# Kernel optimization log

Measured on AMD Instinct MI355X. Metric: run time of the kernel, lower is better.

The kernel has to match this reference:

```python
import jax, jax.numpy as jnp
import numpy as np

DIM = 64      # input/output channels
DIM_K = 16    # key/query dim k
HEADS = 4     # h
U = 1         # intra-depth u
V = DIM // HEADS  # per-head value dim = 16
M = 14        # global context size (D = H = W = M)
REL = 2 * M - 1   # 27
EPS = 1e-5


def _rel_indices(m):
    # positions [n,3], n = m^3; rel_pos[i,j] = pos[j] - pos[i], clamp, shift
    g = np.meshgrid(np.arange(m), np.arange(m), np.arange(m), indexing='ij')
    pos = np.stack(g, axis=-1).reshape(-1, 3)                 # [n,3]
    rel = pos[None, :, :] - pos[:, None, :]                   # [n,n,3]
    rel = np.clip(rel, -m, m) + (m - 1)
    return rel[..., 0], rel[..., 1], rel[..., 2]              # each [n,n]

_D_IDX, _H_IDX, _W_IDX = _rel_indices(M)


def _batchnorm(t, gamma, beta):
    # BatchNorm3d, training mode: per-channel batch stats over (B, D, H, W)
    mean = jnp.mean(t, axis=(0, 2, 3, 4), keepdims=True)
    var = jnp.var(t, axis=(0, 2, 3, 4), keepdims=True)
    tn = (t - mean) * jax.lax.rsqrt(var + EPS)
    return tn * gamma[None, :, None, None, None] + beta[None, :, None, None, None]


def setup_inputs() -> dict:
    key = jax.random.key(0)
    ks = jax.random.split(key, 6)
    B = 4
    x = jax.random.normal(ks[0], (B, DIM, M, M, M), dtype=jnp.float32)
    # 1x1x1 convs == channel matmuls, weight [out_ch, in_ch]
    Wq = jax.random.normal(ks[1], (DIM_K * HEADS, DIM), dtype=jnp.float32) * (DIM_K * DIM) ** (-0.5)
    Wk = jax.random.normal(ks[2], (DIM_K * U, DIM), dtype=jnp.float32) * DIM ** (-0.5)
    Wv = jax.random.normal(ks[3], (V * U, DIM), dtype=jnp.float32) * DIM ** (-0.5)
    rel_pos_emb = jax.random.uniform(ks[4], (REL, REL, REL, DIM_K, U), dtype=jnp.float32)
    gamma_q = jnp.ones((DIM_K * HEADS,), dtype=jnp.float32)
    beta_q = jnp.zeros((DIM_K * HEADS,), dtype=jnp.float32)
    gamma_v = jnp.ones((V * U,), dtype=jnp.float32)
    beta_v = jnp.zeros((V * U,), dtype=jnp.float32)
    return {"x": x, "Wq": Wq, "Wk": Wk, "Wv": Wv, "rel_pos_emb": rel_pos_emb,
            "gamma_q": gamma_q, "beta_q": beta_q, "gamma_v": gamma_v, "beta_v": beta_v}


def reference(x, Wq, Wk, Wv, rel_pos_emb, gamma_q, beta_q, gamma_v, beta_v):
    B, C, D, H, W = x.shape
    n = D * H * W
    q = jnp.einsum('oc,bcdhw->bodhw', Wq, x)
    k = jnp.einsum('oc,bcdhw->bodhw', Wk, x)
    v = jnp.einsum('oc,bcdhw->bodhw', Wv, x)
    q = _batchnorm(q, gamma_q, beta_q)
    v = _batchnorm(v, gamma_v, beta_v)
    q = q.reshape(B, HEADS, DIM_K, n)     # b h k n
    k = k.reshape(B, U, DIM_K, n)         # b u k m
    v = v.reshape(B, U, V, n)             # b u v m
    k = jax.nn.softmax(k, axis=-1)
    # content lambda
    lambda_c = jnp.einsum('bukm,buvm->bkv', k, v)
    y_c = jnp.einsum('bhkn,bkv->bhvn', q, lambda_c)
    # positional lambda via relative-position embedding gather
    rpe = rel_pos_emb[_D_IDX, _H_IDX, _W_IDX]          # [n, n, k, u]
    lambda_p = jnp.einsum('nmku,buvm->bnkv', rpe, v)   # [b, n, k, v]
    y_p = jnp.einsum('bhkn,bnkv->bhvn', q, lambda_p)
    Y = y_c + y_p                                       # [b, h, v, n]
    return Y.reshape(B, HEADS * V, D, H, W)
```

## Files before the change

kernel.cpp:

```cpp
#include <hip/hip_runtime.h>
#include <hip/hip_bf16.h>

#define NPOS 2744
#define BB 4
#define BNTOT (BB*NPOS)
#define RELVOL 19683
#define EROWS2 19688
#define NRT 196
#define NV2 (NRT*2*64)
#define N4T 1024
#define NGRP3 29
#define WDW3 5220

typedef __bf16 bf16x8 __attribute__((ext_vector_type(8)));
typedef float f32x16 __attribute__((ext_vector_type(16)));

#define WS_Q  0u
#define WS_K  2809856u
#define WS_V  3512320u
#define WS_ST 4214784u
#define WS_LA 4216192u
#define WS_LC 4220544u
#define WS_E2 4224640u
#define WS_LP 4856704u
#define WS_VF WS_K

__device__ inline unsigned short f2bf(float f) {
  unsigned int u = __float_as_uint(f);
  return (unsigned short)((u + 0x7fffu + ((u >> 16) & 1u)) >> 16);
}
__device__ inline unsigned int fsh(unsigned int hi, unsigned int lo, int shbits) {
  return (unsigned int)(((((unsigned long long)hi) << 32) | lo) >> shbits);
}
__device__ inline unsigned int pk2(float a, float b) {
  return (unsigned int)f2bf(a) | ((unsigned int)f2bf(b) << 16);
}
__device__ inline float ubf(unsigned int d, int hf) {
  return __uint_as_float(((d >> hf) & 0xFFFFu) << 16);
}

__global__ __launch_bounds__(256) void k_qkv(const float* __restrict__ x,
    const float* __restrict__ Wq, const float* __restrict__ Wk, const float* __restrict__ Wv,
    const float* __restrict__ rpe,
    float* __restrict__ qws, float* __restrict__ kws, float* __restrict__ vws,
    unsigned short* __restrict__ ebf, float* __restrict__ la) {
  int bid = blockIdx.x;
  int tid = threadIdx.x;
  if (bid >= 516) {
    int bid2 = bid - 516;
    if (bid2 == 0 && tid < 272) ((float4*)la)[tid] = make_float4(0.f, 0.f, 0.f, 0.f);
    const int TOT = 16 * EROWS2 + 1024;
    for (int e = bid2 * 256 + tid; e < TOT; e += 308 * 256) {
      if (e < 16 * EROWS2) {
        int k = e / EROWS2;
        int i = e - k * EROWS2;
        float val = (i < RELVOL) ? rpe[i * 16 + k] : 0.f;
        ebf[e] = f2bf(val);
      } else {
        ebf[e] = 0;
      }
    }
    return;
  }
  int cg = bid % 12, nb = bid / 12;
  int gid = nb * 256 + tid;
  if (gid >= BNTOT) return;
  int b = gid / NPOS, n = gid - b * NPOS;
  const float* xp = x + (size_t)b * 64 * NPOS + n;
  int ch0 = cg * 8;
  const float* wbase;
  float* obase;
  if (ch0 < 64)      { wbase = Wq + ch0 * 64;        obase = qws + ((size_t)b * 64 + ch0) * NPOS + n; }
  else if (ch0 < 80) { wbase = Wk + (ch0 - 64) * 64; obase = kws + ((size_t)b * 16 + (ch0 - 64)) * NPOS + n; }
  else               { wbase = Wv + (ch0 - 80) * 64; obase = vws + ((size_t)b * 16 + (ch0 - 80)) * NPOS + n; }

  float acc[8];
#pragma unroll
  for (int j = 0; j < 8; ++j) acc[j] = 0.f;
  for (int c = 0; c < 64; c += 4) {
    float x0 = xp[(c + 0) * NPOS], x1 = xp[(c + 1) * NPOS];
    float x2 = xp[(c + 2) * NPOS], x3 = xp[(c + 3) * NPOS];
#pragma unroll
    for (int j = 0; j < 8; ++j) {
      float4 w = *(const float4*)(wbase + j * 64 + c);
      acc[j] += w.x * x0 + w.y * x1 + w.z * x2 + w.w * x3;
    }
  }
#pragma unroll
  for (int j = 0; j < 8; ++j) obase[(size_t)j * NPOS] = acc[j];
}

__global__ __launch_bounds__(256) void k_sl(const float* __restrict__ qws,
    const float* __restrict__ kws, const float* __restrict__ vws,
    const float* __restrict__ gq, const float* __restrict__ bq,
    const float* __restrict__ gv, const float* __restrict__ bv,
    float* __restrict__ st, float* __restrict__ lcacc) {
  int bid = blockIdx.x;
  int tid = threadIdx.x;
  int wid = tid >> 6;
  __shared__ float red[17][4];
  if (bid < 80) {
    int ch = bid;
    const float* p = (ch < 64) ? (qws + (size_t)ch * NPOS) : (vws + (size_t)(ch - 64) * NPOS);
    size_t pstride = (ch < 64) ? (size_t)64 * NPOS : (size_t)16 * NPOS;
    float s = 0.f, ss = 0.f;
    for (int b = 0; b < 4; ++b) {
      const float* pp = p + b * pstride;
      for (int n = tid; n < NPOS; n += 256) { float v = pp[n]; s += v; ss += v * v; }
    }
#pragma unroll
    for (int o = 32; o > 0; o >>= 1) { s += __shfl_xor(s, o, 64); ss += __shfl_xor(ss, o, 64); }
    if ((tid & 63) == 0) { red[0][wid] = s; red[1][wid] = ss; }
    __syncthreads();
    if (tid == 0) {
      float S = red[0][0] + red[0][1] + red[0][2] + red[0][3];
      float SS = red[1][0] + red[1][1] + red[1][2] + red[1][3];
      float mean = S / (float)BNTOT;
      float var = SS / (float)BNTOT - mean * mean;
      float inv = rsqrtf(var + 1e-5f);
      float g, be;
      if (ch < 64) { g = gq[ch]; be = bq[ch]; } else { g = gv[ch - 64]; be = bv[ch - 64]; }
      float sc = g * inv, sh = be - mean * sc;
      if (ch < 64) { st[ch] = sc; st[64 + ch] = sh; }
      else { st[128 + (ch - 64)] = sc; st[144 + (ch - 64)] = sh; }
    }
  } else {
    int bid2 = bid - 80;
    int b = bid2 >> 6, kc = (bid2 >> 2) & 15, seg = bid2 & 3;
    const float* kp = kws + ((size_t)b * 16 + kc) * NPOS;
    const float* vp = vws + (size_t)b * 16 * NPOS;
    float s = 0.f, acc[16];
#pragma unroll
    for (int v = 0; v < 16; ++v) acc[v] = 0.f;
    int m0 = seg * 686;
    for (int m = m0 + tid; m < m0 + 686; m += 256) {
      float e = __expf(kp[m]);
      s += e;
#pragma unroll
      for (int v = 0; v < 16; ++v) acc[v] += e * vp[(size_t)v * NPOS + m];
    }
#pragma unroll
    for (int o = 32; o > 0; o >>= 1) {
      s += __shfl_xor(s, o, 64);
#pragma unroll
      for (int v = 0; v < 16; ++v) acc[v] += __shfl_xor(acc[v], o, 64);
    }
    if ((tid & 63) == 0) { red[16][wid] = s; for (int v = 0; v < 16; ++v) red[v][wid] = acc[v]; }
    __syncthreads();
    if (tid < 17) {
      float tot = red[tid][0] + red[tid][1] + red[tid][2] + red[tid][3];
      atomicAdd(lcacc + ((size_t)b * 16 + kc) * 17 + tid, tot);
    }
  }
}

__global__ __launch_bounds__(256) void k_conv2(const float* __restrict__ vws,
    const float* __restrict__ st, const float* __restrict__ lcacc,
    uint4* __restrict__ vfrag, float* __restrict__ lc) {
  int idx = blockIdx.x * 256 + threadIdx.x;
  if (idx < NV2) {
    int rt = idx >> 7; int r = idx & 127;
    int ct = r >> 6, l = r & 63;
    int zm = rt / 14, ym = rt - zm * 14;
    int kh = l >> 5;
    int b = ct * 2 + ((l >> 4) & 1), v = l & 15;
    int mrow = zm * 196 + ym * 14;
    float sc = st[128 + v], sh = st[144 + v];
    unsigned int wds[4];
#pragma unroll
    for (int i = 0; i < 4; ++i) {
      int x0 = kh * 8 + 2 * i, x1 = x0 + 1;
      float f0 = 0.f, f1 = 0.f;
      if (x0 < 14) f0 = vws[((size_t)b * 16 + v) * NPOS + mrow + x0] * sc + sh;
      if (x1 < 14) f1 = vws[((size_t)b * 16 + v) * NPOS + mrow + x1] * sc + sh;
      wds[i] = (unsigned int)f2bf(f0) | ((unsigned int)f2bf(f1) << 16);
    }
    vfrag[(rt * 2 + ct) * 64 + l] = make_uint4(wds[0], wds[1], wds[2], wds[3]);
  } else if (idx < NV2 + N4T) {
    int t = idx - NV2;
    int b = t >> 8, kc = (t >> 4) & 15, v = t & 15;
    const float* la = lcacc + ((size_t)b * 16 + kc) * 17;
    float S = la[16];
    lc[((size_t)b * 16 + kc) * 16 + v] = st[128 + v] * (la[v] / S) + st[144 + v];
  }
}

__global__ __launch_bounds__(256, 3) void k_lam(const unsigned short* __restrict__ ebf,
    const uint4* __restrict__ vfrag, unsigned int* __restrict__ lpb) {
  __shared__ unsigned int lds[12320];
  int tid = threadIdx.x;
  int w = tid >> 6, l = tid & 63;
  int bid = blockIdx.x;
  int k = bid / NGRP3, ng = bid - k * NGRP3;
  int n0 = ng * 96;
  int nmax = min(n0 + 95, NPOS - 1);
  int zx = nmax / 196, tx = nmax - zx * 196, yx = tx / 14, xx = tx - yx * 14;
  int b0 = (9841 - (zx * 729 + yx * 27 + xx)) & ~7;

  const unsigned int* gsrc = (const unsigned int*)(ebf + (size_t)k * EROWS2 + b0);
#pragma unroll
  for (int it = 0; it < 6; ++it) {
    int ck = it * 256 + tid;
    if (ck < WDW3 / 4) {
      uint4 g = *(const uint4*)(gsrc + 4 * ck);
      unsigned int g4 = gsrc[4 * ck + 4];
      *(uint4*)(&lds[4 * ck]) = g;
      uint4 h;
      h.x = fsh(g.y, g.x, 16); h.y = fsh(g.z, g.y, 16);
      h.z = fsh(g.w, g.z, 16); h.w = fsh(g4, g.w, 16);
      *(uint4*)(&lds[WDW3 + 4 * ck]) = h;
    }
  }
  int i = l & 31, kh = l >> 5;
  int n_a = min(n0 + i, NPOS - 1);
  int n_b = min(n0 + 32 + i, NPOS - 1);
  int n_c = min(n0 + 64 + i, NPOS - 1);
  int za = n_a / 196, ta = n_a - za * 196, ya = ta / 14, xa = ta - ya * 14;
  int zb = n_b / 196, tb = n_b - zb * 196, yb = tb / 14, xb = tb - yb * 14;
  int zc = n_c / 196, tc = n_c - zc * 196, yc = tc / 14, xc = tc - yc * 14;
  int soff0 = 9841 - (za * 729 + ya * 27 + xa) - b0 + kh * 8;
  int soff1 = 9841 - (zb * 729 + yb * 27 + xb) - b0 + kh * 8;
  int soff2 = 9841 - (zc * 729 + yc * 27 + xc) - b0 + kh * 8;
  __syncthreads();

  f32x16 a0c0, a0c1, a1c0, a1c1, a2c0, a2c1;
#pragma unroll
  for (int q = 0; q < 16; ++q) {
    a0c0[q] = 0.f; a0c1[q] = 0.f; a1c0[q] = 0.f;
    a1c1[q] = 0.f; a2c0[q] = 0.f; a2c1[q] = 0.f;
  }

  int rtS = w * 49;
  int zm = rtS / 14, ym = rtS - zm * 14;
  int crel = zm * 729 + ym * 27;
  const uint4* vfp = vfrag + (size_t)(rtS * 2) * 64 + l;
  uint4 B0 = vfp[0], B1 = vfp[64];
  for (int d = 0; d < 49; ++d) {
    const uint4* vfn = vfp + ((d < 48) ? 128 : 0);
    uint4 nB0 = vfn[0], nB1 = vfn[64];
    int o0 = soff0 + crel, o1 = soff1 + crel, o2 = soff2 + crel;
    int ad0 = (o0 >> 1) + (o0 & 1) * WDW3;
    int ad1 = (o1 >> 1) + (o1 & 1) * WDW3;
    int ad2 = (o2 >> 1) + (o2 & 1) * WDW3;
    uint4 A0 = make_uint4(lds[ad0], lds[ad0 + 1], lds[ad0 + 2], lds[ad0 + 3]);
    uint4 A1 = make_uint4(lds[ad1], lds[ad1 + 1], lds[ad1 + 2], lds[ad1 + 3]);
    uint4 A2 = make_uint4(lds[ad2], lds[ad2 + 1], lds[ad2 + 2], lds[ad2 + 3]);
    __builtin_amdgcn_s_setprio(1);
    a0c0 = __builtin_amdgcn_mfma_f32_32x32x16_bf16(
        __builtin_bit_cast(bf16x8, A0), __builtin_bit_cast(bf16x8, B0), a0c0, 0, 0, 0);
    a0c1 = __builtin_amdgcn_mfma_f32_32x32x16_bf16(
        __builtin_bit_cast(bf16x8, A0), __builtin_bit_cast(bf16x8, B1), a0c1, 0, 0, 0);
    a1c0 = __builtin_amdgcn_mfma_f32_32x32x16_bf16(
        __builtin_bit_cast(bf16x8, A1), __builtin_bit_cast(bf16x8, B0), a1c0, 0, 0, 0);
    a1c1 = __builtin_amdgcn_mfma_f32_32x32x16_bf16(
        __builtin_bit_cast(bf16x8, A1), __builtin_bit_cast(bf16x8, B1), a1c1, 0, 0, 0);
    a2c0 = __builtin_amdgcn_mfma_f32_32x32x16_bf16(
        __builtin_bit_cast(bf16x8, A2), __builtin_bit_cast(bf16x8, B0), a2c0, 0, 0, 0);
    a2c1 = __builtin_amdgcn_mfma_f32_32x32x16_bf16(
        __builtin_bit_cast(bf16x8, A2), __builtin_bit_cast(bf16x8, B1), a2c1, 0, 0, 0);
    __builtin_amdgcn_s_setprio(0);
    B0 = nB0; B1 = nB1; vfp = vfn;
    ++ym;
    if (ym == 14) { ym = 0; crel += 378; } else { crel += 27; }
  }

  __syncthreads();
  float* red = (float*)lds;
  if (w >= 2) {
    float* r0 = red + (w - 2) * 6144;
#pragma unroll
    for (int r = 0; r < 16; ++r) {
      r0[r * 64 + l] = a0c0[r];          r0[1024 + r * 64 + l] = a0c1[r];
      r0[2048 + r * 64 + l] = a1c0[r];   r0[3072 + r * 64 + l] = a1c1[r];
      r0[4096 + r * 64 + l] = a2c0[r];   r0[5120 + r * 64 + l] = a2c1[r];
    }
  }
  __syncthreads();
  if (w < 2) {
    const float* r0 = red + w * 6144;
#pragma unroll
    for (int r = 0; r < 16; ++r) {
      a0c0[r] += r0[r * 64 + l];         a0c1[r] += r0[1024 + r * 64 + l];
      a1c0[r] += r0[2048 + r * 64 + l];  a1c1[r] += r0[3072 + r * 64 + l];
      a2c0[r] += r0[4096 + r * 64 + l];  a2c1[r] += r0[5120 + r * 64 + l];
    }
  }
  __syncthreads();
  if (w == 1) {
#pragma unroll
    for (int r = 0; r < 16; ++r) {
      red[r * 64 + l] = a0c0[r];          red[1024 + r * 64 + l] = a0c1[r];
      red[2048 + r * 64 + l] = a1c0[r];   red[3072 + r * 64 + l] = a1c1[r];
      red[4096 + r * 64 + l] = a2c0[r];   red[5120 + r * 64 + l] = a2c1[r];
    }
  }
  __syncthreads();
  if (w == 0) {
#pragma unroll
    for (int r = 0; r < 16; ++r) {
      a0c0[r] += red[r * 64 + l];         a0c1[r] += red[1024 + r * 64 + l];
      a1c0[r] += red[2048 + r * 64 + l];  a1c1[r] += red[3072 + r * 64 + l];
      a2c0[r] += red[4096 + r * 64 + l];  a2c1[r] += red[5120 + r * 64 + l];
    }
    float* fl = (float*)lds;
    int bv0 = ((l >> 4) & 1) * 16 + (l & 15);
#define DUMP(ACC, NT, CT)                                                   \
    {                                                                       \
_Pragma("unroll")                                                           \
      for (int r = 0; r < 16; ++r) {                                        \
        int nl = (NT) * 32 + ((r & 3) + 8 * (r >> 2) + 4 * kh);             \
        fl[nl * 64 + (CT) * 32 + bv0] = ACC[r];                             \
      }                                                                     \
    }
    DUMP(a0c0, 0, 0) DUMP(a0c1, 0, 1)
    DUMP(a1c0, 1, 0) DUMP(a1c1, 1, 1)
    DUMP(a2c0, 2, 0) DUMP(a2c1, 2, 1)
#undef DUMP
  }
  __syncthreads();
  {
    const float* fl = (const float*)lds;
#pragma unroll
    for (int it = 0; it < 12; ++it) {
      int idx = it * 256 + tid;
      int vd = idx & 7, b = (idx >> 3) & 3, nl = idx >> 5;
      int n = n0 + nl;
      if (n < NPOS) {
        float2 f = *(const float2*)&fl[nl * 64 + b * 16 + 2 * vd];
        lpb[((size_t)(b * NPOS + n) * 16 + k) * 8 + vd] = pk2(f.x, f.y);
      }
    }
  }
}

__global__ __launch_bounds__(128) void k_ep(const unsigned int* __restrict__ lpb,
    const float* __restrict__ qws, const float* __restrict__ st,
    const float* __restrict__ lc, float* __restrict__ out) {
  __shared__ unsigned int laml[32 * 130];
  __shared__ float qlds[64 * 33];
  __shared__ float lclds[256];
  int tid = threadIdx.x;
  int bid = blockIdx.x;
  int b = bid & 3, chk = bid >> 2;
  int n0 = chk * 32;
  const uint4* lsrc = (const uint4*)(lpb + (size_t)(b * NPOS + n0) * 128);
#pragma unroll
  for (int it = 0; it < 8; ++it) {
    int idx4 = it * 128 + tid;
    uint4 g = lsrc[idx4];
    int n_loc = idx4 >> 5, rem = (idx4 & 31) * 4;
    unsigned int* d = &laml[n_loc * 130 + rem];
    d[0] = g.x; d[1] = g.y; d[2] = g.z; d[3] = g.w;
  }
  const float* qb = qws + (size_t)b * 64 * NPOS + n0;
#pragma unroll
  for (int it = 0; it < 4; ++it) {
    int idx4 = it * 128 + tid;
    int ch = idx4 >> 3, c4 = (idx4 & 7) * 4;
    float4 g = *(const float4*)(qb + (size_t)ch * NPOS + c4);
    float sc = st[ch], sh = st[64 + ch];
    float* d = &qlds[ch * 33 + c4];
    d[0] = g.x * sc + sh; d[1] = g.y * sc + sh;
    d[2] = g.z * sc + sh; d[3] = g.w * sc + sh;
  }
  lclds[tid] = lc[b * 256 + tid];
  lclds[128 + tid] = lc[b * 256 + 128 + tid];
  __syncthreads();
  int vq = tid & 3, n_loc = tid >> 2;
  int n = n0 + n_loc;
  if (n >= NPOS) return;
  float y[16];
#pragma unroll
  for (int i = 0; i < 16; ++i) y[i] = 0.f;
#pragma unroll
  for (int k = 0; k < 16; ++k) {
    uint2 lp = *(const uint2*)&laml[n_loc * 130 + k * 8 + vq * 2];
    const float* lcr = &lclds[k * 16 + vq * 4];
    float l0 = ubf(lp.x, 0) + lcr[0];
    float l1 = ubf(lp.x, 16) + lcr[1];
    float l2 = ubf(lp.y, 0) + lcr[2];
    float l3 = ubf(lp.y, 16) + lcr[3];
#pragma unroll
    for (int h = 0; h < 4; ++h) {
      float q = qlds[(h * 16 + k) * 33 + n_loc];
      y[h * 4 + 0] += q * l0; y[h * 4 + 1] += q * l1;
      y[h * 4 + 2] += q * l2; y[h * 4 + 3] += q * l3;
    }
  }
  size_t ob = ((size_t)b * 64 + vq * 4) * NPOS + n;
#pragma unroll
  for (int h = 0; h < 4; ++h)
#pragma unroll
    for (int j = 0; j < 4; ++j)
      out[ob + (size_t)(h * 16 + j) * NPOS] = y[h * 4 + j];
}

extern "C" void kernel_launch(void* const* d_in, const int* in_sizes, int n_in,
                              void* d_out, int out_size, void* d_ws, size_t ws_size,
                              hipStream_t stream) {
  const float* x   = (const float*)d_in[0];
  const float* Wq  = (const float*)d_in[1];
  const float* Wk  = (const float*)d_in[2];
  const float* Wv  = (const float*)d_in[3];
  const float* rpe = (const float*)d_in[4];
  const float* gq  = (const float*)d_in[5];
  const float* bq  = (const float*)d_in[6];
  const float* gv  = (const float*)d_in[7];
  const float* bv  = (const float*)d_in[8];
  float* out = (float*)d_out;
  char* ws = (char*)d_ws;
  float* qws = (float*)(ws + WS_Q);
  float* kws = (float*)(ws + WS_K);
  float* vws = (float*)(ws + WS_V);
  float* st  = (float*)(ws + WS_ST);
  float* la  = (float*)(ws + WS_LA);
  float* lcp = (float*)(ws + WS_LC);
  unsigned short* ebf = (unsigned short*)(ws + WS_E2);
  unsigned int* lpb = (unsigned int*)(ws + WS_LP);
  uint4* vfrag = (uint4*)(ws + WS_VF);

  k_qkv<<<824, 256, 0, stream>>>(x, Wq, Wk, Wv, rpe, qws, kws, vws, ebf, la);
  k_sl<<<336, 256, 0, stream>>>(qws, kws, vws, gq, bq, gv, bv, st, la);
  k_conv2<<<102, 256, 0, stream>>>(vws, st, la, vfrag, lcp);
  k_lam<<<16 * NGRP3, 256, 0, stream>>>(ebf, vfrag, lpb);
  k_ep<<<344, 128, 0, stream>>>(lpb, qws, st, lcp, out);
}
```

Before: 60.92 us.

## Split k_lam reduction over m into two halves with smaller n tiles

k_lam now tiles n by 64 instead of 96 and splits the m (source position) range into two halves handled by separate blocks. Each block stages a smaller LDS window of the embedding, which allows 4 blocks per CU and 1376 blocks instead of 464. Block ids are remapped in an XCD-aware order. The two partial lambda_p results are written to separate halves of the workspace as bf16 and summed in k_ep. This adds an extra bf16 rounding step and doubles lpb traffic in exchange for more parallelism and occupancy.

```diff
diff --git a/kernel.cpp b/kernel.cpp
--- a/kernel.cpp
+++ b/kernel.cpp
@@ -9,8 +9,9 @@
 #define NRT 196
 #define NV2 (NRT*2*64)
 #define N4T 1024
-#define NGRP3 29
-#define WDW3 5220
+#define NGRP 43
+#define WDWH 2688
+#define HALFDW ((size_t)4*NPOS*16*8)
 
 typedef __bf16 bf16x8 __attribute__((ext_vector_type(8)));
 typedef float f32x16 __attribute__((ext_vector_type(16)));
@@ -37,6 +38,9 @@
 }
 __device__ inline float ubf(unsigned int d, int hf) {
   return __uint_as_float(((d >> hf) & 0xFFFFu) << 16);
+}
+__device__ inline unsigned int addpk(unsigned int a, unsigned int b) {
+  return pk2(ubf(a, 0) + ubf(b, 0), ubf(a, 16) + ubf(b, 16));
 }
 
 __global__ __launch_bounds__(256) void k_qkv(const float* __restrict__ x,
@@ -185,79 +189,72 @@
   }
 }
 
-__global__ __launch_bounds__(256, 3) void k_lam(const unsigned short* __restrict__ ebf,
+__global__ __launch_bounds__(256, 4) void k_lam(const unsigned short* __restrict__ ebf,
     const uint4* __restrict__ vfrag, unsigned int* __restrict__ lpb) {
-  __shared__ unsigned int lds[12320];
+  __shared__ unsigned int lds[5412];
   int tid = threadIdx.x;
   int w = tid >> 6, l = tid & 63;
-  int bid = blockIdx.x;
-  int k = bid / NGRP3, ng = bid - k * NGRP3;
-  int n0 = ng * 96;
-  int nmax = min(n0 + 95, NPOS - 1);
+  int orig = blockIdx.x;
+  int bid = (orig & 7) * 172 + (orig >> 3);
+  int mh = bid & 1, kb = bid >> 1;
+  int k = kb / NGRP, ng = kb - k * NGRP;
+  int n0 = ng * 64;
+  int crowbase = 5103 * mh;
+  int nmax = min(n0 + 63, NPOS - 1);
   int zx = nmax / 196, tx = nmax - zx * 196, yx = tx / 14, xx = tx - yx * 14;
-  int b0 = (9841 - (zx * 729 + yx * 27 + xx)) & ~7;
+  int b0 = (9841 - (zx * 729 + yx * 27 + xx) + crowbase) & ~7;
 
   const unsigned int* gsrc = (const unsigned int*)(ebf + (size_t)k * EROWS2 + b0);
 #pragma unroll
-  for (int it = 0; it < 6; ++it) {
+  for (int it = 0; it < 3; ++it) {
     int ck = it * 256 + tid;
-    if (ck < WDW3 / 4) {
+    if (ck < WDWH / 4) {
       uint4 g = *(const uint4*)(gsrc + 4 * ck);
       unsigned int g4 = gsrc[4 * ck + 4];
       *(uint4*)(&lds[4 * ck]) = g;
       uint4 h;
       h.x = fsh(g.y, g.x, 16); h.y = fsh(g.z, g.y, 16);
       h.z = fsh(g.w, g.z, 16); h.w = fsh(g4, g.w, 16);
-      *(uint4*)(&lds[WDW3 + 4 * ck]) = h;
+      *(uint4*)(&lds[WDWH + 4 * ck]) = h;
     }
   }
   int i = l & 31, kh = l >> 5;
   int n_a = min(n0 + i, NPOS - 1);
   int n_b = min(n0 + 32 + i, NPOS - 1);
-  int n_c = min(n0 + 64 + i, NPOS - 1);
   int za = n_a / 196, ta = n_a - za * 196, ya = ta / 14, xa = ta - ya * 14;
   int zb = n_b / 196, tb = n_b - zb * 196, yb = tb / 14, xb = tb - yb * 14;
-  int zc = n_c / 196, tc = n_c - zc * 196, yc = tc / 14, xc = tc - yc * 14;
-  int soff0 = 9841 - (za * 729 + ya * 27 + xa) - b0 + kh * 8;
-  int soff1 = 9841 - (zb * 729 + yb * 27 + xb) - b0 + kh * 8;
-  int soff2 = 9841 - (zc * 729 + yc * 27 + xc) - b0 + kh * 8;
+  int soff0 = 9841 - (za * 729 + ya * 27 + xa) + crowbase - b0 + kh * 8;
+  int soff1 = 9841 - (zb * 729 + yb * 27 + xb) + crowbase - b0 + kh * 8;
   __syncthreads();
 
-  f32x16 a0c0, a0c1, a1c0, a1c1, a2c0, a2c1;
-#pragma unroll
-  for (int q = 0; q < 16; ++q) {
-    a0c0[q] = 0.f; a0c1[q] = 0.f; a1c0[q] = 0.f;
-    a1c1[q] = 0.f; a2c0[q] = 0.f; a2c1[q] = 0.f;
-  }
-
-  int rtS = w * 49;
+  f32x16 ac00, ac01, ac10, ac11;
+#pragma unroll
+  for (int q = 0; q < 16; ++q) { ac00[q] = 0.f; ac01[q] = 0.f; ac10[q] = 0.f; ac11[q] = 0.f; }
+
+  const int stw[5] = {0, 25, 50, 74, 98};
+  int rtS = mh * 98 + stw[w];
+  int cnt = stw[w + 1] - stw[w];
   int zm = rtS / 14, ym = rtS - zm * 14;
-  int crel = zm * 729 + ym * 27;
+  int crel = (zm - 7 * mh) * 729 + ym * 27;
   const uint4* vfp = vfrag + (size_t)(rtS * 2) * 64 + l;
   uint4 B0 = vfp[0], B1 = vfp[64];
-  for (int d = 0; d < 49; ++d) {
-    const uint4* vfn = vfp + ((d < 48) ? 128 : 0);
+  for (int d = 0; d < cnt; ++d) {
+    const uint4* vfn = vfp + ((d < cnt - 1) ? 128 : 0);
     uint4 nB0 = vfn[0], nB1 = vfn[64];
-    int o0 = soff0 + crel, o1 = soff1 + crel, o2 = soff2 + crel;
-    int ad0 = (o0 >> 1) + (o0 & 1) * WDW3;
-    int ad1 = (o1 >> 1) + (o1 & 1) * WDW3;
-    int ad2 = (o2 >> 1) + (o2 & 1) * WDW3;
+    int o0 = soff0 + crel, o1 = soff1 + crel;
+    int ad0 = (o0 >> 1) + (o0 & 1) * WDWH;
+    int ad1 = (o1 >> 1) + (o1 & 1) * WDWH;
     uint4 A0 = make_uint4(lds[ad0], lds[ad0 + 1], lds[ad0 + 2], lds[ad0 + 3]);
     uint4 A1 = make_uint4(lds[ad1], lds[ad1 + 1], lds[ad1 + 2], lds[ad1 + 3]);
-    uint4 A2 = make_uint4(lds[ad2], lds[ad2 + 1], lds[ad2 + 2], lds[ad2 + 3]);
     __builtin_amdgcn_s_setprio(1);
-    a0c0 = __builtin_amdgcn_mfma_f32_32x32x16_bf16(
-        __builtin_bit_cast(bf16x8, A0), __builtin_bit_cast(bf16x8, B0), a0c0, 0, 0, 0);
-    a0c1 = __builtin_amdgcn_mfma_f32_32x32x16_bf16(
-        __builtin_bit_cast(bf16x8, A0), __builtin_bit_cast(bf16x8, B1), a0c1, 0, 0, 0);
-    a1c0 = __builtin_amdgcn_mfma_f32_32x32x16_bf16(
-        __builtin_bit_cast(bf16x8, A1), __builtin_bit_cast(bf16x8, B0), a1c0, 0, 0, 0);
-    a1c1 = __builtin_amdgcn_mfma_f32_32x32x16_bf16(
-        __builtin_bit_cast(bf16x8, A1), __builtin_bit_cast(bf16x8, B1), a1c1, 0, 0, 0);
-    a2c0 = __builtin_amdgcn_mfma_f32_32x32x16_bf16(
-        __builtin_bit_cast(bf16x8, A2), __builtin_bit_cast(bf16x8, B0), a2c0, 0, 0, 0);
-    a2c1 = __builtin_amdgcn_mfma_f32_32x32x16_bf16(
-        __builtin_bit_cast(bf16x8, A2), __builtin_bit_cast(bf16x8, B1), a2c1, 0, 0, 0);
+    ac00 = __builtin_amdgcn_mfma_f32_32x32x16_bf16(
+        __builtin_bit_cast(bf16x8, A0), __builtin_bit_cast(bf16x8, B0), ac00, 0, 0, 0);
+    ac01 = __builtin_amdgcn_mfma_f32_32x32x16_bf16(
+        __builtin_bit_cast(bf16x8, A0), __builtin_bit_cast(bf16x8, B1), ac01, 0, 0, 0);
+    ac10 = __builtin_amdgcn_mfma_f32_32x32x16_bf16(
+        __builtin_bit_cast(bf16x8, A1), __builtin_bit_cast(bf16x8, B0), ac10, 0, 0, 0);
+    ac11 = __builtin_amdgcn_mfma_f32_32x32x16_bf16(
+        __builtin_bit_cast(bf16x8, A1), __builtin_bit_cast(bf16x8, B1), ac11, 0, 0, 0);
     __builtin_amdgcn_s_setprio(0);
     B0 = nB0; B1 = nB1; vfp = vfn;
     ++ym;
@@ -266,42 +263,26 @@
 
   __syncthreads();
   float* red = (float*)lds;
-  if (w >= 2) {
-    float* r0 = red + (w - 2) * 6144;
-#pragma unroll
-    for (int r = 0; r < 16; ++r) {
-      r0[r * 64 + l] = a0c0[r];          r0[1024 + r * 64 + l] = a0c1[r];
-      r0[2048 + r * 64 + l] = a1c0[r];   r0[3072 + r * 64 + l] = a1c1[r];
-      r0[4096 + r * 64 + l] = a2c0[r];   r0[5120 + r * 64 + l] = a2c1[r];
-    }
-  }
-  __syncthreads();
-  if (w < 2) {
-    const float* r0 = red + w * 6144;
-#pragma unroll
-    for (int r = 0; r < 16; ++r) {
-      a0c0[r] += r0[r * 64 + l];         a0c1[r] += r0[1024 + r * 64 + l];
-      a1c0[r] += r0[2048 + r * 64 + l];  a1c1[r] += r0[3072 + r * 64 + l];
-      a2c0[r] += r0[4096 + r * 64 + l];  a2c1[r] += r0[5120 + r * 64 + l];
-    }
-  }
-  __syncthreads();
-  if (w == 1) {
-#pragma unroll
-    for (int r = 0; r < 16; ++r) {
-      red[r * 64 + l] = a0c0[r];          red[1024 + r * 64 + l] = a0c1[r];
-      red[2048 + r * 64 + l] = a1c0[r];   red[3072 + r * 64 + l] = a1c1[r];
-      red[4096 + r * 64 + l] = a2c0[r];   red[5120 + r * 64 + l] = a2c1[r];
-    }
-  }
-  __syncthreads();
+#pragma unroll
+  for (int src = 1; src < 4; ++src) {
+    if (w == src) {
+#pragma unroll
+      for (int r = 0; r < 16; ++r) {
+        red[r * 64 + l] = ac00[r];          red[1024 + r * 64 + l] = ac01[r];
+        red[2048 + r * 64 + l] = ac10[r];   red[3072 + r * 64 + l] = ac11[r];
+      }
+    }
+    __syncthreads();
+    if (w == 0) {
+#pragma unroll
+      for (int r = 0; r < 16; ++r) {
+        ac00[r] += red[r * 64 + l];         ac01[r] += red[1024 + r * 64 + l];
+        ac10[r] += red[2048 + r * 64 + l];  ac11[r] += red[3072 + r * 64 + l];
+      }
+    }
+    __syncthreads();
+  }
   if (w == 0) {
-#pragma unroll
-    for (int r = 0; r < 16; ++r) {
-      a0c0[r] += red[r * 64 + l];         a0c1[r] += red[1024 + r * 64 + l];
-      a1c0[r] += red[2048 + r * 64 + l];  a1c1[r] += red[3072 + r * 64 + l];
-      a2c0[r] += red[4096 + r * 64 + l];  a2c1[r] += red[5120 + r * 64 + l];
-    }
     float* fl = (float*)lds;
     int bv0 = ((l >> 4) & 1) * 16 + (l & 15);
 #define DUMP(ACC, NT, CT)                                                   \
@@ -312,22 +293,21 @@
         fl[nl * 64 + (CT) * 32 + bv0] = ACC[r];                             \
       }                                                                     \
     }
-    DUMP(a0c0, 0, 0) DUMP(a0c1, 0, 1)
-    DUMP(a1c0, 1, 0) DUMP(a1c1, 1, 1)
-    DUMP(a2c0, 2, 0) DUMP(a2c1, 2, 1)
+    DUMP(ac00, 0, 0) DUMP(ac01, 0, 1)
+    DUMP(ac10, 1, 0) DUMP(ac11, 1, 1)
 #undef DUMP
   }
   __syncthreads();
   {
     const float* fl = (const float*)lds;
 #pragma unroll
-    for (int it = 0; it < 12; ++it) {
+    for (int it = 0; it < 8; ++it) {
       int idx = it * 256 + tid;
       int vd = idx & 7, b = (idx >> 3) & 3, nl = idx >> 5;
       int n = n0 + nl;
       if (n < NPOS) {
         float2 f = *(const float2*)&fl[nl * 64 + b * 16 + 2 * vd];
-        lpb[((size_t)(b * NPOS + n) * 16 + k) * 8 + vd] = pk2(f.x, f.y);
+        lpb[(size_t)mh * HALFDW + ((size_t)(b * NPOS + n) * 16 + k) * 8 + vd] = pk2(f.x, f.y);
       }
     }
   }
@@ -344,13 +324,16 @@
   int b = bid & 3, chk = bid >> 2;
   int n0 = chk * 32;
   const uint4* lsrc = (const uint4*)(lpb + (size_t)(b * NPOS + n0) * 128);
+  const uint4* lsrc2 = lsrc + (HALFDW >> 2);
 #pragma unroll
   for (int it = 0; it < 8; ++it) {
     int idx4 = it * 128 + tid;
-    uint4 g = lsrc[idx4];
+    uint4 g0 = lsrc[idx4];
+    uint4 g1 = lsrc2[idx4];
     int n_loc = idx4 >> 5, rem = (idx4 & 31) * 4;
     unsigned int* d = &laml[n_loc * 130 + rem];
-    d[0] = g.x; d[1] = g.y; d[2] = g.z; d[3] = g.w;
+    d[0] = addpk(g0.x, g1.x); d[1] = addpk(g0.y, g1.y);
+    d[2] = addpk(g0.z, g1.z); d[3] = addpk(g0.w, g1.w);
   }
   const float* qb = qws + (size_t)b * 64 * NPOS + n0;
 #pragma unroll
@@ -422,6 +405,6 @@
   k_qkv<<<824, 256, 0, stream>>>(x, Wq, Wk, Wv, rpe, qws, kws, vws, ebf, la);
   k_sl<<<336, 256, 0, stream>>>(qws, kws, vws, gq, bq, gv, bv, st, la);
   k_conv2<<<102, 256, 0, stream>>>(vws, st, la, vfrag, lcp);
-  k_lam<<<16 * NGRP3, 256, 0, stream>>>(ebf, vfrag, lpb);
+  k_lam<<<16 * NGRP * 2, 256, 0, stream>>>(ebf, vfrag, lpb);
   k_ep<<<344, 128, 0, stream>>>(lpb, qws, st, lcp, out);
 }
```

After: 64.29 us. 1.06x slower.
